# Optimization experiments

Hardware: AMD Instinct MI355X
Metric: run time of the kernel (lower is better)

## Reference

```python
import jax, jax.numpy as jnp
import numpy as np

N_NODES = 50000
N_EDGES = 800000
DIM_IN = 128
DIM_OUT = 64


def setup_inputs() -> dict:
    key = jax.random.key(0)
    k1, k2, k3, k4 = jax.random.split(key, 4)
    x = jax.random.normal(k1, (N_NODES, DIM_IN), dtype=jnp.float32)
    edge_index = jax.random.randint(k2, (2, N_EDGES), 0, N_NODES, dtype=jnp.int64)
    W = jax.random.normal(k3, (DIM_IN, DIM_OUT), dtype=jnp.float32) / np.sqrt(DIM_IN)
    b = jax.random.normal(k4, (DIM_OUT,), dtype=jnp.float32) * 0.01
    return {"x": x, "edge_index": edge_index, "W": W, "b": b}


def reference(x, edge_index, W, b):
    # Faithful PyG GCNConv: add self-loops, symmetric deg normalization,
    # linear transform then normalized scatter-add aggregation, then bias.
    N = x.shape[0]
    h = x @ W  # [N, dim_out] — transform before propagate (PyG order)

    loops = jnp.arange(N, dtype=edge_index.dtype)
    src = jnp.concatenate([edge_index[0], loops])  # [E+N]
    dst = jnp.concatenate([edge_index[1], loops])  # [E+N]

    ones = jnp.ones(src.shape[0], dtype=h.dtype)
    deg = jax.ops.segment_sum(ones, dst, num_segments=N)  # in-degree incl. self-loop
    dinv = jnp.where(deg > 0, jax.lax.rsqrt(deg), 0.0)
    norm = dinv[src] * dinv[dst]  # [E+N]

    msgs = h[src] * norm[:, None]  # gather + scale
    out = jax.ops.segment_sum(msgs, dst, num_segments=N) + b  # scatter-add
    return jax.nn.log_softmax(out, axis=1)
```

## Files before the change

### kernel.cpp

```cpp
#include <hip/hip_runtime.h>
#include <hip/hip_fp16.h>
#include <cstdint>
#include <cstddef>

#define N_NODES 50000
#define N_EDGES 800000
#define DIM_IN  128
#define DIM_OUT 64

#define B2SHIFT 8
#define B2NODES 256
#define NB2     ((N_NODES + B2NODES - 1) / B2NODES)
#define EB      4096
#define SORTB   ((N_EDGES + EB - 1) / EB)
#define NE4     (N_EDGES / 4)
#define CAPB    4864
#define GROWS   128
#define GEMMB   ((N_NODES + GROWS - 1) / GROWS)
#define GPAD    16
#define NEGRP   ((N_NODES + 31) / 32)

typedef _Float16 f16x8 __attribute__((ext_vector_type(8)));
typedef float    f32x4 __attribute__((ext_vector_type(4)));

__global__ __launch_bounds__(256) void k_zero(int* __restrict__ gcnt) {
    const int i = blockIdx.x * 256 + threadIdx.x;
    if (i < NB2 * GPAD) gcnt[i] = 0;
}

__global__ __launch_bounds__(256) void kFG(const int* __restrict__ ei,
                                           int* __restrict__ gcnt,
                                           unsigned* __restrict__ pairs,
                                           const float* __restrict__ x,
                                           const float* __restrict__ W,
                                           __half* __restrict__ h) {
    const int t = threadIdx.x;
    if (blockIdx.x < SORTB) {
        __shared__ int hcnt[B2NODES];
        __shared__ int cur[B2NODES];
        const int blk = blockIdx.x;
        hcnt[t] = 0;
        __syncthreads();
        const int4* src4 = (const int4*)ei;
        const int4* dst4 = (const int4*)(ei + N_EDGES);
        const int g0 = blk * (EB / 4);
#pragma unroll
        for (int it = 0; it < EB / 1024; ++it) {
            const int g = g0 + it * 256 + t;
            if (g < NE4) {
                const int4 d = dst4[g];
                atomicAdd(&hcnt[d.x >> B2SHIFT], 1);
                atomicAdd(&hcnt[d.y >> B2SHIFT], 1);
                atomicAdd(&hcnt[d.z >> B2SHIFT], 1);
                atomicAdd(&hcnt[d.w >> B2SHIFT], 1);
            }
        }
        __syncthreads();
        {
            const int c = hcnt[t];
            const int base = c ? atomicAdd(&gcnt[t * GPAD], c) : 0;
            cur[t] = t * CAPB + base;
        }
        __syncthreads();
#pragma unroll
        for (int it = 0; it < EB / 1024; ++it) {
            const int g = g0 + it * 256 + t;
            if (g < NE4) {
                const int4 sv = src4[g];
                const int4 dv = dst4[g];
                int b, p;
                b = dv.x >> B2SHIFT; p = atomicAdd(&cur[b], 1);
                if (p < b * CAPB + CAPB) pairs[p] = ((unsigned)sv.x << 16) | (unsigned)dv.x;
                b = dv.y >> B2SHIFT; p = atomicAdd(&cur[b], 1);
                if (p < b * CAPB + CAPB) pairs[p] = ((unsigned)sv.y << 16) | (unsigned)dv.y;
                b = dv.z >> B2SHIFT; p = atomicAdd(&cur[b], 1);
                if (p < b * CAPB + CAPB) pairs[p] = ((unsigned)sv.z << 16) | (unsigned)dv.z;
                b = dv.w >> B2SHIFT; p = atomicAdd(&cur[b], 1);
                if (p < b * CAPB + CAPB) pairs[p] = ((unsigned)sv.w << 16) | (unsigned)dv.w;
            }
        }
    } else {
        const int u = blockIdx.x - SORTB;
        const int w = t >> 6;
        const int l = t & 63;
        const int q = l >> 4;
        const int m16 = l & 15;

        f16x8 bf[4][4];
#pragma unroll
        for (int kc = 0; kc < 4; ++kc)
#pragma unroll
            for (int ct = 0; ct < 4; ++ct) {
                const float* wp = W + (size_t)(kc * 32 + q * 8) * DIM_OUT + ct * 16 + m16;
                f16x8 v;
#pragma unroll
                for (int j = 0; j < 8; ++j) v[j] = (_Float16)wp[(size_t)j * DIM_OUT];
                bf[kc][ct] = v;
            }

        const int base = u * GROWS + w * 32;
#pragma unroll
        for (int rt = 0; rt < 2; ++rt) {
            const int m0 = base + rt * 16;
            int mrow = m0 + m16;
            if (mrow >= N_NODES) mrow = N_NODES - 1;

            f16x8 af[4];
#pragma unroll
            for (int kc = 0; kc < 4; ++kc) {
                const float4* xp = (const float4*)(x + (size_t)mrow * DIM_IN + kc * 32 + q * 8);
                const float4 p0 = xp[0], p1 = xp[1];
                f16x8 a;
                a[0] = (_Float16)p0.x; a[1] = (_Float16)p0.y;
                a[2] = (_Float16)p0.z; a[3] = (_Float16)p0.w;
                a[4] = (_Float16)p1.x; a[5] = (_Float16)p1.y;
                a[6] = (_Float16)p1.z; a[7] = (_Float16)p1.w;
                af[kc] = a;
            }

            f32x4 acc[4];
#pragma unroll
            for (int ct = 0; ct < 4; ++ct) acc[ct] = (f32x4){0.f, 0.f, 0.f, 0.f};
#pragma unroll
            for (int kc = 0; kc < 4; ++kc)
#pragma unroll
                for (int ct = 0; ct < 4; ++ct)
                    acc[ct] = __builtin_amdgcn_mfma_f32_16x16x32_f16(af[kc], bf[kc][ct], acc[ct], 0, 0, 0);

#pragma unroll
            for (int reg = 0; reg < 4; ++reg) {
                const int r = m0 + q * 4 + reg;
                if (r < N_NODES) {
#pragma unroll
                    for (int ct = 0; ct < 4; ++ct)
                        h[(size_t)r * DIM_OUT + ct * 16 + m16] = __float2half(acc[ct][reg]);
                }
            }
        }
    }
}

__global__ __launch_bounds__(512) void kSort(const unsigned* __restrict__ pairs,
                                             const int* __restrict__ gcnt,
                                             unsigned short* __restrict__ csr,
                                             int2* __restrict__ nodeoff2,
                                             __half* __restrict__ h) {
    __shared__ int cnt[B2NODES];
    __shared__ int cur[B2NODES];
    __shared__ float sdinv[B2NODES];
    __shared__ int wsum[4];
    __shared__ unsigned short lcsr[CAPB];
    const int b = blockIdx.x, t = threadIdx.x;
    const int eb = b * CAPB;
    const int count = min(gcnt[b * GPAD], CAPB);
    const int ee = eb + count;

    if (t < B2NODES) cnt[t] = 0;
    __syncthreads();

    {
        int i = eb + t;
        for (; i + 1536 < ee; i += 2048) {
            const unsigned p0 = pairs[i];
            const unsigned p1 = pairs[i + 512];
            const unsigned p2 = pairs[i + 1024];
            const unsigned p3 = pairs[i + 1536];
            atomicAdd(&cnt[p0 & (B2NODES - 1)], 1);
            atomicAdd(&cnt[p1 & (B2NODES - 1)], 1);
            atomicAdd(&cnt[p2 & (B2NODES - 1)], 1);
            atomicAdd(&cnt[p3 & (B2NODES - 1)], 1);
        }
        for (; i < ee; i += 512) atomicAdd(&cnt[pairs[i] & (B2NODES - 1)], 1);
    }
    __syncthreads();

    if (t < B2NODES) {
        const int lane = t & 63;
        const int v = cnt[t];
        int xs = v;
#pragma unroll
        for (int off = 1; off < 64; off <<= 1) {
            int y = __shfl_up(xs, off);
            if (lane >= off) xs += y;
        }
        cur[t] = xs;
        if (lane == 63) wsum[t >> 6] = xs;
    }
    __syncthreads();
    if (t == 0) {
        int acc = 0;
#pragma unroll
        for (int w2 = 0; w2 < 4; ++w2) { const int v2 = wsum[w2]; wsum[w2] = acc; acc += v2; }
    }
    __syncthreads();
    if (t < B2NODES) {
        const int v = cnt[t];
        const int excl = cur[t] - v + wsum[t >> 6];
        sdinv[t] = rsqrtf((float)(v + 1));
        const int n = (b << B2SHIFT) + t;
        if (n < N_NODES) nodeoff2[n] = make_int2(eb + excl, v);
        cur[t] = excl;
    }
    __syncthreads();

    for (int i = eb + t; i < ee; i += 512) {
        const unsigned p = pairs[i];
        const int q = atomicAdd(&cur[p & (B2NODES - 1)], 1);
        lcsr[q] = (unsigned short)(p >> 16);
    }
    __syncthreads();

    {
        const int cw = (count + 1) >> 1;
        const unsigned* l32 = (const unsigned*)lcsr;
        unsigned* c32 = (unsigned*)(csr + eb);
        for (int i2 = t; i2 < cw; i2 += 512) c32[i2] = l32[i2];
    }
    {
        f16x8* h8w = (f16x8*)h;
        for (int idx = t; idx < B2NODES * 8; idx += 512) {
            const int r = idx >> 3;
            const int n = (b << B2SHIFT) + r;
            if (n < N_NODES) {
                const float d = sdinv[r];
                f16x8 v = h8w[(size_t)n * 8 + (idx & 7)];
#pragma unroll
                for (int j = 0; j < 8; ++j) v[j] = (_Float16)((float)v[j] * d);
                h8w[(size_t)n * 8 + (idx & 7)] = v;
            }
        }
    }
}

__global__ __launch_bounds__(256) void kE_agg(const int2* __restrict__ nodeoff2,
                                              const unsigned short* __restrict__ csr,
                                              const __half* __restrict__ h,
                                              const float* __restrict__ bvec,
                                              float* __restrict__ out) {
    const int t = threadIdx.x;
    const int ew = t >> 3, sl = t & 7;
    const int n = blockIdx.x * 32 + ew;
    if (n >= N_NODES) return;
    const f16x8* __restrict__ h8 = (const f16x8*)h;

    const int2 off = nodeoff2[n];
    const int s0 = off.x, s1 = off.x + off.y;

    const f16x8 hv = h8[(size_t)n * 8 + sl];
    float a[8];
#pragma unroll
    for (int j = 0; j < 8; ++j) a[j] = (float)hv[j];

    int i = s0;
    for (; i + 4 <= s1; i += 4) {
        const int c0 = csr[i + 0];
        const int c1 = csr[i + 1];
        const int c2 = csr[i + 2];
        const int c3 = csr[i + 3];
        const f16x8 v0 = h8[(size_t)c0 * 8 + sl];
        const f16x8 v1 = h8[(size_t)c1 * 8 + sl];
        const f16x8 v2 = h8[(size_t)c2 * 8 + sl];
        const f16x8 v3 = h8[(size_t)c3 * 8 + sl];
#pragma unroll
        for (int j = 0; j < 8; ++j)
            a[j] += (float)v0[j] + (float)v1[j] + (float)v2[j] + (float)v3[j];
    }
    for (; i < s1; ++i) {
        const f16x8 v0 = h8[(size_t)csr[i] * 8 + sl];
#pragma unroll
        for (int j = 0; j < 8; ++j) a[j] += (float)v0[j];
    }

    const float4 b0 = *(const float4*)&bvec[8 * sl];
    const float4 b1 = *(const float4*)&bvec[8 * sl + 4];
    const float di = rsqrtf((float)(off.y + 1));
    float v[8];
    v[0] = a[0] * di + b0.x; v[1] = a[1] * di + b0.y;
    v[2] = a[2] * di + b0.z; v[3] = a[3] * di + b0.w;
    v[4] = a[4] * di + b1.x; v[5] = a[5] * di + b1.y;
    v[6] = a[6] * di + b1.z; v[7] = a[7] * di + b1.w;

    float m = v[0];
#pragma unroll
    for (int j = 1; j < 8; ++j) m = fmaxf(m, v[j]);
#pragma unroll
    for (int o = 4; o > 0; o >>= 1) m = fmaxf(m, __shfl_xor(m, o));
    float s = 0.f;
#pragma unroll
    for (int j = 0; j < 8; ++j) s += __expf(v[j] - m);
#pragma unroll
    for (int o = 4; o > 0; o >>= 1) s += __shfl_xor(s, o);
    const float ls = m + __logf(s);

    float4 o0, o1;
    o0.x = v[0] - ls; o0.y = v[1] - ls; o0.z = v[2] - ls; o0.w = v[3] - ls;
    o1.x = v[4] - ls; o1.y = v[5] - ls; o1.z = v[6] - ls; o1.w = v[7] - ls;
    *(float4*)&out[(size_t)n * DIM_OUT + 8 * sl]     = o0;
    *(float4*)&out[(size_t)n * DIM_OUT + 8 * sl + 4] = o1;
}

extern "C" void kernel_launch(void* const* d_in, const int* in_sizes, int n_in,
                              void* d_out, int out_size, void* d_ws, size_t ws_size,
                              hipStream_t stream) {
    const float* x  = (const float*)d_in[0];
    const int*   ei = (const int*)d_in[1];
    const float* W  = (const float*)d_in[2];
    const float* b  = (const float*)d_in[3];
    float* out = (float*)d_out;

    char* ws = (char*)d_ws;
    __half*         h        = (__half*)ws;         ws += (size_t)N_NODES * DIM_OUT * sizeof(__half);
    unsigned*       pairs    = (unsigned*)ws;       ws += (size_t)NB2 * CAPB * sizeof(unsigned);
    unsigned short* csr      = (unsigned short*)ws; ws += (size_t)NB2 * CAPB * sizeof(unsigned short);
    int2*           nodeoff2 = (int2*)ws;           ws += (size_t)N_NODES * sizeof(int2);
    int*            gcnt     = (int*)ws;            ws += (size_t)NB2 * GPAD * sizeof(int);

    k_zero <<<(NB2 * GPAD + 255) / 256, 256, 0, stream>>>(gcnt);
    kFG    <<<SORTB + GEMMB, 256, 0, stream>>>(ei, gcnt, pairs, x, W, h);
    kSort  <<<NB2, 512, 0, stream>>>(pairs, gcnt, csr, nodeoff2, h);
    kE_agg <<<NEGRP, 256, 0, stream>>>(nodeoff2, csr, h, b, out);
}
```

Baseline: 114.2 us.

## Batch edge loads in binning, unroll aggregation by 8, memset counters

The binning phase now loads all src/dst int4 vectors up front and keeps them in registers, so the scatter pass no longer reloads them. Its atomics are split from the stores to allow more memory-level parallelism. The aggregation kernel gains an 8-way unrolled gather loop to keep more neighbor loads in flight, and the zeroing kernel is replaced by hipMemsetAsync. Register pressure rises in both kernels, which may lower occupancy.

Result: no change. 114.6 us, median of 2 (+0.3%).

```diff
diff --git a/kernel.cpp b/kernel.cpp
--- a/kernel.cpp
+++ b/kernel.cpp
@@ -22,11 +22,6 @@
 
 typedef _Float16 f16x8 __attribute__((ext_vector_type(8)));
 typedef float    f32x4 __attribute__((ext_vector_type(4)));
-
-__global__ __launch_bounds__(256) void k_zero(int* __restrict__ gcnt) {
-    const int i = blockIdx.x * 256 + threadIdx.x;
-    if (i < NB2 * GPAD) gcnt[i] = 0;
-}
 
 __global__ __launch_bounds__(256) void kFG(const int* __restrict__ ei,
                                            int* __restrict__ gcnt,
@@ -44,15 +39,22 @@
         const int4* src4 = (const int4*)ei;
         const int4* dst4 = (const int4*)(ei + N_EDGES);
         const int g0 = blk * (EB / 4);
-#pragma unroll
-        for (int it = 0; it < EB / 1024; ++it) {
+
+        int4 dv[4], sv[4];
+        bool live[4];
+#pragma unroll
+        for (int it = 0; it < 4; ++it) {
             const int g = g0 + it * 256 + t;
-            if (g < NE4) {
-                const int4 d = dst4[g];
-                atomicAdd(&hcnt[d.x >> B2SHIFT], 1);
-                atomicAdd(&hcnt[d.y >> B2SHIFT], 1);
-                atomicAdd(&hcnt[d.z >> B2SHIFT], 1);
-                atomicAdd(&hcnt[d.w >> B2SHIFT], 1);
+            live[it] = (g < NE4);
+            if (live[it]) { dv[it] = dst4[g]; sv[it] = src4[g]; }
+        }
+#pragma unroll
+        for (int it = 0; it < 4; ++it) {
+            if (live[it]) {
+                atomicAdd(&hcnt[dv[it].x >> B2SHIFT], 1);
+                atomicAdd(&hcnt[dv[it].y >> B2SHIFT], 1);
+                atomicAdd(&hcnt[dv[it].z >> B2SHIFT], 1);
+                atomicAdd(&hcnt[dv[it].w >> B2SHIFT], 1);
             }
         }
         __syncthreads();
@@ -62,21 +64,35 @@
             cur[t] = t * CAPB + base;
         }
         __syncthreads();
-#pragma unroll
-        for (int it = 0; it < EB / 1024; ++it) {
-            const int g = g0 + it * 256 + t;
-            if (g < NE4) {
-                const int4 sv = src4[g];
-                const int4 dv = dst4[g];
-                int b, p;
-                b = dv.x >> B2SHIFT; p = atomicAdd(&cur[b], 1);
-                if (p < b * CAPB + CAPB) pairs[p] = ((unsigned)sv.x << 16) | (unsigned)dv.x;
-                b = dv.y >> B2SHIFT; p = atomicAdd(&cur[b], 1);
-                if (p < b * CAPB + CAPB) pairs[p] = ((unsigned)sv.y << 16) | (unsigned)dv.y;
-                b = dv.z >> B2SHIFT; p = atomicAdd(&cur[b], 1);
-                if (p < b * CAPB + CAPB) pairs[p] = ((unsigned)sv.z << 16) | (unsigned)dv.z;
-                b = dv.w >> B2SHIFT; p = atomicAdd(&cur[b], 1);
-                if (p < b * CAPB + CAPB) pairs[p] = ((unsigned)sv.w << 16) | (unsigned)dv.w;
+        {
+            int pos[16];
+            int bb[16];
+#pragma unroll
+            for (int it = 0; it < 4; ++it) {
+                if (live[it]) {
+                    bb[it * 4 + 0] = dv[it].x >> B2SHIFT;
+                    bb[it * 4 + 1] = dv[it].y >> B2SHIFT;
+                    bb[it * 4 + 2] = dv[it].z >> B2SHIFT;
+                    bb[it * 4 + 3] = dv[it].w >> B2SHIFT;
+#pragma unroll
+                    for (int c2 = 0; c2 < 4; ++c2)
+                        pos[it * 4 + c2] = atomicAdd(&cur[bb[it * 4 + c2]], 1);
+                }
+            }
+#pragma unroll
+            for (int it = 0; it < 4; ++it) {
+                if (live[it]) {
+                    const int p0 = pos[it * 4 + 0], p1 = pos[it * 4 + 1];
+                    const int p2 = pos[it * 4 + 2], p3 = pos[it * 4 + 3];
+                    if (p0 < bb[it * 4 + 0] * CAPB + CAPB)
+                        pairs[p0] = ((unsigned)sv[it].x << 16) | (unsigned)dv[it].x;
+                    if (p1 < bb[it * 4 + 1] * CAPB + CAPB)
+                        pairs[p1] = ((unsigned)sv[it].y << 16) | (unsigned)dv[it].y;
+                    if (p2 < bb[it * 4 + 2] * CAPB + CAPB)
+                        pairs[p2] = ((unsigned)sv[it].z << 16) | (unsigned)dv[it].z;
+                    if (p3 < bb[it * 4 + 3] * CAPB + CAPB)
+                        pairs[p3] = ((unsigned)sv[it].w << 16) | (unsigned)dv[it].w;
+                }
             }
         }
     } else {
@@ -252,6 +268,18 @@
     for (int j = 0; j < 8; ++j) a[j] = (float)hv[j];
 
     int i = s0;
+    for (; i + 8 <= s1; i += 8) {
+        int c[8];
+        f16x8 v[8];
+#pragma unroll
+        for (int j = 0; j < 8; ++j) c[j] = csr[i + j];
+#pragma unroll
+        for (int j = 0; j < 8; ++j) v[j] = h8[(size_t)c[j] * 8 + sl];
+#pragma unroll
+        for (int j = 0; j < 8; ++j)
+#pragma unroll
+            for (int k = 0; k < 8; ++k) a[k] += (float)v[j][k];
+    }
     for (; i + 4 <= s1; i += 4) {
         const int c0 = csr[i + 0];
         const int c1 = csr[i + 1];
@@ -315,7 +343,7 @@
     int2*           nodeoff2 = (int2*)ws;           ws += (size_t)N_NODES * sizeof(int2);
     int*            gcnt     = (int*)ws;            ws += (size_t)NB2 * GPAD * sizeof(int);
 
-    k_zero <<<(NB2 * GPAD + 255) / 256, 256, 0, stream>>>(gcnt);
+    hipMemsetAsync(gcnt, 0, (size_t)NB2 * GPAD * sizeof(int), stream);
     kFG    <<<SORTB + GEMMB, 256, 0, stream>>>(ei, gcnt, pairs, x, W, h);
     kSort  <<<NB2, 512, 0, stream>>>(pairs, gcnt, csr, nodeoff2, h);
     kE_agg <<<NEGRP, 256, 0, stream>>>(nodeoff2, csr, h, b, out);
```
